# Kernel tuning notes

Hardware: AMD Instinct MI355X
Metric: run time of the kernel (lower is better)

Reference implementation:

```python
import jax, jax.numpy as jnp
import numpy as np

NUM_FEATURES = 602
NUM_CLASSES = 41
HIDDEN = 8
HEADS1 = 8
HEADS2 = 1
N_NODES = 100000
N_EDGES = 1600000
NEG_SLOPE = 0.2  # PyG GATConv default leaky_relu slope
EPS = 1e-16      # PyG softmax denominator epsilon


def gat_conv(x, edge_index, W, att_src, att_dst, bias, heads, out_ch, concat):
    """Faithful PyG GATConv forward (eval mode, dropout disabled).
    x: [N, F_in], edge_index: [2, E] with row0=src, row1=dst.
    W: [F_in, heads*out_ch], att_src/att_dst: [heads, out_ch], bias: [heads*out_ch] or [out_ch].
    """
    N = x.shape[0]
    h = (x @ W).reshape(N, heads, out_ch)              # [N, H, C]
    a_src = jnp.einsum('nhc,hc->nh', h, att_src)       # [N, H]
    a_dst = jnp.einsum('nhc,hc->nh', h, att_dst)       # [N, H]
    src, dst = edge_index[0], edge_index[1]
    e = jax.nn.leaky_relu(a_src[src] + a_dst[dst], NEG_SLOPE)  # [E, H]
    # segment softmax over incoming edges of each dst node
    m = jax.ops.segment_max(e, dst, num_segments=N)    # [N, H]
    e = jnp.exp(e - m[dst])
    denom = jax.ops.segment_sum(e, dst, num_segments=N)  # [N, H]
    alpha = e / (denom[dst] + EPS)                     # [E, H]
    msg = h[src] * alpha[:, :, None]                   # [E, H, C]
    out = jax.ops.segment_sum(msg, dst, num_segments=N)  # [N, H, C]
    if concat:
        out = out.reshape(N, heads * out_ch)
    else:
        out = out.mean(axis=1)
    return out + bias


def setup_inputs() -> dict:
    key = jax.random.key(0)
    ks = jax.random.split(key, 10)
    x = jax.random.normal(ks[0], (N_NODES, NUM_FEATURES), dtype=jnp.float32)
    edge_index = jax.random.randint(ks[1], (2, N_EDGES), 0, N_NODES, dtype=jnp.int64)
    s = 0.1
    W1 = jax.random.normal(ks[2], (NUM_FEATURES, HEADS1 * HIDDEN), dtype=jnp.float32) * s
    att_src1 = jax.random.normal(ks[3], (HEADS1, HIDDEN), dtype=jnp.float32) * s
    att_dst1 = jax.random.normal(ks[4], (HEADS1, HIDDEN), dtype=jnp.float32) * s
    b1 = jnp.zeros((HEADS1 * HIDDEN,), dtype=jnp.float32)
    W2 = jax.random.normal(ks[5], (HEADS1 * HIDDEN, HEADS2 * NUM_CLASSES), dtype=jnp.float32) * s
    att_src2 = jax.random.normal(ks[6], (HEADS2, NUM_CLASSES), dtype=jnp.float32) * s
    att_dst2 = jax.random.normal(ks[7], (HEADS2, NUM_CLASSES), dtype=jnp.float32) * s
    b2 = jnp.zeros((NUM_CLASSES,), dtype=jnp.float32)
    return {"x": x, "edge_index": edge_index, "W1": W1, "att_src1": att_src1,
            "att_dst1": att_dst1, "b1": b1, "W2": W2, "att_src2": att_src2,
            "att_dst2": att_dst2, "b2": b2}


def reference(x, edge_index, W1, att_src1, att_dst1, b1, W2, att_src2, att_dst2, b2):
    # eval mode: all F.dropout calls are identity
    h = gat_conv(x, edge_index, W1, att_src1, att_dst1, b1, HEADS1, HIDDEN, concat=True)
    h = jax.nn.elu(h)
    h = gat_conv(h, edge_index, W2, att_src2, att_dst2, b2, HEADS2, NUM_CLASSES, concat=False)
    return jax.nn.log_softmax(h, axis=1)
```

## Files before the change

kernel.cpp:

```cpp
#include <hip/hip_runtime.h>
#include <math.h>

#define NN 100000
#define NE 1600000
#define F_IN 602
#define H1 8
#define C1 8
#define F_MID 64
#define NC 41
#define H2_LD 48
#define NEG_SLOPE 0.2f
#define WT_LD 640
#define GB1 ((NN + 63) / 64)
#define DGB 1024
#define ATB ((NN * H1 + 255) / 256)

#define LRELU(x) fmaxf((x), NEG_SLOPE * (x))

typedef __attribute__((ext_vector_type(8))) short short8;
typedef __attribute__((ext_vector_type(4))) float f32x4;

__device__ inline unsigned short f2bf(float f) {
    unsigned u = __builtin_bit_cast(unsigned, f);
    unsigned r = (u + 0x7FFFu + ((u >> 16) & 1u)) >> 16;
    return (unsigned short)r;
}
__device__ inline float bf2f(unsigned short u) {
    unsigned v = ((unsigned)u) << 16;
    return __builtin_bit_cast(float, v);
}

__global__ void zero_kernel(int4* __restrict__ p, int n4)
{
    int i = blockIdx.x * blockDim.x + threadIdx.x;
    if (i < n4) p[i] = make_int4(0, 0, 0, 0);
}

__global__ void prep_wt_kernel(const float* __restrict__ W, unsigned short* __restrict__ Wt)
{
    int idx = blockIdx.x * blockDim.x + threadIdx.x;
    if (idx >= F_MID * WT_LD) return;
    int col = idx / WT_LD, k = idx % WT_LD;
    Wt[idx] = (k < F_IN) ? f2bf(W[k * F_MID + col]) : (unsigned short)0;
}

__global__ __launch_bounds__(256) void mega1_kernel(
    const float* __restrict__ x, const unsigned short* __restrict__ Wt,
    unsigned short* __restrict__ h1b,
    const int* __restrict__ dst, int* __restrict__ deg, int* __restrict__ rank,
    int N, int E)
{
    __shared__ unsigned short As[64][40];
    __shared__ unsigned short Bs[64][40];

    int bid = blockIdx.x;
    int t = threadIdx.x;

    if (bid < DGB) {
        for (int e = bid * 256 + t; e < E; e += DGB * 256)
            rank[e] = atomicAdd(&deg[dst[e]], 1);
        return;
    }

    int lane = t & 63;
    int w = t >> 6;
    int l16 = lane & 15, lg = lane >> 4;
    int n0 = (bid - DGB) * 64;

    int arow = t >> 2, aseg = t & 3;
    int grow = n0 + arow;
    const float* xrow = x + (size_t)(grow < N ? grow : 0) * F_IN + aseg * 8;
    int bcol = t >> 2;
    const unsigned short* wrow = Wt + (size_t)bcol * WT_LD + aseg * 8;

    f32x4 acc[4] = {};
    float2 av[4];
    uint4  bv;

    #pragma unroll
    for (int i = 0; i < 4; ++i) av[i] = *(const float2*)(xrow + i * 2);
    bv = *(const uint4*)(wrow);

    for (int kt = 0; kt < 19; ++kt) {
        __syncthreads();
        {
            unsigned short tmp[8];
            #pragma unroll
            for (int i = 0; i < 4; ++i) {
                tmp[i * 2]     = f2bf(av[i].x);
                tmp[i * 2 + 1] = f2bf(av[i].y);
            }
            *(uint4*)(&As[arow][aseg * 8]) = *(uint4*)tmp;
            *(uint4*)(&Bs[bcol][aseg * 8]) = bv;
        }
        __syncthreads();

        if (kt < 18) {
            int k0 = (kt + 1) * 32;
            if (kt + 1 < 18) {
                #pragma unroll
                for (int i = 0; i < 4; ++i) av[i] = *(const float2*)(xrow + k0 + i * 2);
            } else {
                #pragma unroll
                for (int i = 0; i < 4; ++i) {
                    int k = k0 + aseg * 8 + i * 2;
                    float a = (k < F_IN)     ? xrow[k0 + i * 2]     : 0.f;
                    float b = (k + 1 < F_IN) ? xrow[k0 + i * 2 + 1] : 0.f;
                    av[i] = make_float2(a, b);
                }
            }
            bv = *(const uint4*)(wrow + k0);
        }

        short8 afrag = *(const short8*)(&As[w * 16 + l16][lg * 8]);
        short8 bfrag[4];
        #pragma unroll
        for (int n = 0; n < 4; ++n)
            bfrag[n] = *(const short8*)(&Bs[n * 16 + l16][lg * 8]);
        #pragma unroll
        for (int n = 0; n < 4; ++n)
            acc[n] = __builtin_amdgcn_mfma_f32_16x16x32_bf16(afrag, bfrag[n], acc[n], 0, 0, 0);
    }

    #pragma unroll
    for (int r = 0; r < 4; ++r) {
        int row = n0 + w * 16 + lg * 4 + r;
        if (row < N) {
            #pragma unroll
            for (int n = 0; n < 4; ++n)
                h1b[(size_t)row * F_MID + n * 16 + l16] = f2bf(acc[n][r]);
        }
    }
}

__global__ void scan1_kernel(const int* __restrict__ deg, int* __restrict__ bsum, int N)
{
    int b = blockIdx.x, t = threadIdx.x;
    int base = b * 1024 + t * 16;
    int s = 0;
    #pragma unroll
    for (int i = 0; i < 16; ++i) { int idx = base + i; if (idx < N) s += deg[idx]; }
    #pragma unroll
    for (int o = 32; o > 0; o >>= 1) s += __shfl_down(s, o);
    if (t == 0) bsum[b] = s;
}

__global__ void scan2_kernel(const int* __restrict__ bsum, int* __restrict__ boff,
                             int nb, int* __restrict__ offs, int N, int E)
{
    __shared__ int buf[128];
    int t = threadIdx.x;
    int v = (t < nb) ? bsum[t] : 0;
    buf[t] = v;
    __syncthreads();
    for (int o = 1; o < 128; o <<= 1) {
        int u = (t >= o) ? buf[t - o] : 0;
        __syncthreads();
        buf[t] += u;
        __syncthreads();
    }
    if (t < nb) boff[t] = buf[t] - v;
    if (t == 0) offs[N] = E;
}

__global__ void scan3_kernel(const int* __restrict__ deg, const int* __restrict__ boff,
                             int* __restrict__ offs, int N)
{
    int b = blockIdx.x, t = threadIdx.x;
    int base = b * 1024 + t * 16;
    int loc[16];
    int s = 0;
    #pragma unroll
    for (int i = 0; i < 16; ++i) {
        int idx = base + i;
        loc[i] = (idx < N) ? deg[idx] : 0;
        s += loc[i];
    }
    int inc = s;
    #pragma unroll
    for (int o = 1; o < 64; o <<= 1) {
        int u = __shfl_up(inc, o);
        if (t >= o) inc += u;
    }
    int run = inc - s + boff[b];
    #pragma unroll
    for (int i = 0; i < 16; ++i) {
        int idx = base + i;
        if (idx < N) offs[idx] = run;
        run += loc[i];
    }
}

__global__ void mega2_kernel(
    const unsigned short* __restrict__ h1b,
    const float* __restrict__ attS, const float* __restrict__ attD,
    float* __restrict__ asrc, float* __restrict__ adst,
    const int* __restrict__ src, const int* __restrict__ dst,
    const int* __restrict__ rank, const int* __restrict__ offs,
    int* __restrict__ srcs, int N, int E)
{
    int bid = blockIdx.x, t = threadIdx.x;
    if (bid < DGB) {
        for (int e = bid * 256 + t; e < E; e += DGB * 256)
            srcs[offs[dst[e]] + rank[e]] = src[e];
        return;
    }
    int idx = (bid - DGB) * 256 + t;
    if (idx >= N * H1) return;
    int n = idx >> 3, hh = idx & 7;
    float s = 0.f, d = 0.f;
    #pragma unroll
    for (int c = 0; c < C1; ++c) {
        float v = bf2f(h1b[n * F_MID + hh * C1 + c]);
        s += v * attS[hh * C1 + c];
        d += v * attD[hh * C1 + c];
    }
    asrc[idx] = s;
    adst[idx] = d;
}

__global__ void agg1_kernel(const int* __restrict__ offs, const int* __restrict__ srcs,
                            const unsigned short* __restrict__ h1b,
                            const float* __restrict__ asrc, const float* __restrict__ adst,
                            const float* __restrict__ b1,
                            float* __restrict__ out1, int N)
{
    int wave = (blockIdx.x * blockDim.x + threadIdx.x) >> 6;
    int lane = threadIdx.x & 63;
    if (wave >= N) return;
    int n = wave;
    int hh = lane >> 3;
    int beg = offs[n], end = offs[n + 1];
    float ad = adst[n * H1 + hh];

    float m = -INFINITY, den = 0.f, acc = 0.f;
    int i = beg;
    for (; i + 8 <= end; i += 8) {
        int s[8];
        #pragma unroll
        for (int j = 0; j < 8; ++j) s[j] = srcs[i + j];
        float a[8], v[8];
        #pragma unroll
        for (int j = 0; j < 8; ++j) a[j] = asrc[s[j] * H1 + hh];
        #pragma unroll
        for (int j = 0; j < 8; ++j) v[j] = bf2f(h1b[(size_t)s[j] * F_MID + lane]);
        float e[8];
        #pragma unroll
        for (int j = 0; j < 8; ++j) e[j] = LRELU(a[j] + ad);
        float m8 = fmaxf(fmaxf(fmaxf(e[0], e[1]), fmaxf(e[2], e[3])),
                         fmaxf(fmaxf(e[4], e[5]), fmaxf(e[6], e[7])));
        float mn = fmaxf(m, m8);
        float sc = __expf(m - mn);
        float p[8];
        #pragma unroll
        for (int j = 0; j < 8; ++j) p[j] = __expf(e[j] - mn);
        den = den * sc + (((p[0] + p[1]) + (p[2] + p[3])) + ((p[4] + p[5]) + (p[6] + p[7])));
        acc = acc * sc + (((p[0] * v[0] + p[1] * v[1]) + (p[2] * v[2] + p[3] * v[3]))
                        + ((p[4] * v[4] + p[5] * v[5]) + (p[6] * v[6] + p[7] * v[7])));
        m = mn;
    }
    for (; i < end; ++i) {
        int s = srcs[i];
        float e = LRELU(asrc[s * H1 + hh] + ad);
        float hv = bf2f(h1b[(size_t)s * F_MID + lane]);
        float mn = fmaxf(m, e);
        float sc = __expf(m - mn);
        float p  = __expf(e - mn);
        den = den * sc + p;
        acc = acc * sc + p * hv;
        m = mn;
    }
    float inv = 1.f / (den + 1e-16f);
    float v = acc * inv + b1[lane];
    out1[n * F_MID + lane] = v > 0.f ? v : expm1f(v);
}

__global__ __launch_bounds__(256) void gemm2_kernel(
    const float* __restrict__ out1, const float* __restrict__ W2,
    float* __restrict__ h2p, int N)
{
    __shared__ float ws[F_MID * NC];
    for (int i = threadIdx.x; i < F_MID * NC; i += 256) ws[i] = W2[i];
    __syncthreads();
    int idx = blockIdx.x * blockDim.x + threadIdx.x;
    if (idx >= N * NC) return;
    int n = idx / NC, j = idx % NC;
    const float* row = out1 + n * F_MID;
    float acc = 0.f;
    #pragma unroll
    for (int k = 0; k < F_MID; ++k) acc += row[k] * ws[k * NC + j];
    h2p[(size_t)n * H2_LD + j] = acc;
}

__global__ void attn2_kernel(float* __restrict__ h2p,
                             const float* __restrict__ attS,
                             const float* __restrict__ attD,
                             float* __restrict__ adst, int N)
{
    int n = blockIdx.x * blockDim.x + threadIdx.x;
    if (n >= N) return;
    float s = 0.f, d = 0.f;
    #pragma unroll
    for (int j = 0; j < NC; ++j) {
        float v = h2p[(size_t)n * H2_LD + j];
        s += v * attS[j];
        d += v * attD[j];
    }
    h2p[(size_t)n * H2_LD + NC] = s;
    adst[n] = d;
}

__global__ void agg2_kernel(const int* __restrict__ offs, const int* __restrict__ srcs,
                            const float* __restrict__ h2p,
                            const float* __restrict__ adst,
                            const float* __restrict__ b2,
                            float* __restrict__ out, int N)
{
    int wave = (blockIdx.x * blockDim.x + threadIdx.x) >> 6;
    int lane = threadIdx.x & 63;
    if (wave >= N) return;
    int n = wave;
    int beg = offs[n], end = offs[n + 1];
    float ad = adst[n];
    bool act = lane < NC;
    int li = act ? lane : NC;

    float m = -INFINITY, den = 0.f, acc = 0.f;
    int i = beg;
    for (; i + 8 <= end; i += 8) {
        int s[8];
        #pragma unroll
        for (int j = 0; j < 8; ++j) s[j] = srcs[i + j];
        float hv[8];
        #pragma unroll
        for (int j = 0; j < 8; ++j) hv[j] = h2p[(size_t)s[j] * H2_LD + li];
        float a[8];
        #pragma unroll
        for (int j = 0; j < 8; ++j) a[j] = __shfl(hv[j], NC);
        float e[8];
        #pragma unroll
        for (int j = 0; j < 8; ++j) e[j] = LRELU(a[j] + ad);
        float m8 = fmaxf(fmaxf(fmaxf(e[0], e[1]), fmaxf(e[2], e[3])),
                         fmaxf(fmaxf(e[4], e[5]), fmaxf(e[6], e[7])));
        float mn = fmaxf(m, m8);
        float sc = __expf(m - mn);
        float p[8];
        #pragma unroll
        for (int j = 0; j < 8; ++j) p[j] = __expf(e[j] - mn);
        den = den * sc + (((p[0] + p[1]) + (p[2] + p[3])) + ((p[4] + p[5]) + (p[6] + p[7])));
        acc = acc * sc + (((p[0] * hv[0] + p[1] * hv[1]) + (p[2] * hv[2] + p[3] * hv[3]))
                        + ((p[4] * hv[4] + p[5] * hv[5]) + (p[6] * hv[6] + p[7] * hv[7])));
        m = mn;
    }
    for (; i < end; ++i) {
        int s = srcs[i];
        float hv = h2p[(size_t)s * H2_LD + li];
        float a = __shfl(hv, NC);
        float e = LRELU(a + ad);
        float mn = fmaxf(m, e);
        float sc = __expf(m - mn);
        float p  = __expf(e - mn);
        den = den * sc + p;
        acc = acc * sc + p * hv;
        m = mn;
    }
    float inv = 1.f / (den + 1e-16f);
    float v = act ? acc * inv + b2[lane] : -INFINITY;
    float mm = v;
    #pragma unroll
    for (int o = 32; o > 0; o >>= 1) mm = fmaxf(mm, __shfl_xor(mm, o));
    float ex = act ? __expf(v - mm) : 0.f;
    float S = ex;
    #pragma unroll
    for (int o = 32; o > 0; o >>= 1) S += __shfl_xor(S, o);
    if (act) out[n * NC + lane] = v - mm - logf(S);
}

extern "C" void kernel_launch(void* const* d_in, const int* in_sizes, int n_in,
                              void* d_out, int out_size, void* d_ws, size_t ws_size,
                              hipStream_t stream)
{
    const float* x     = (const float*)d_in[0];
    const int*   ei    = (const int*)  d_in[1];
    const float* W1    = (const float*)d_in[2];
    const float* attS1 = (const float*)d_in[3];
    const float* attD1 = (const float*)d_in[4];
    const float* b1    = (const float*)d_in[5];
    const float* W2    = (const float*)d_in[6];
    const float* attS2 = (const float*)d_in[7];
    const float* attD2 = (const float*)d_in[8];
    const float* b2    = (const float*)d_in[9];
    float* out = (float*)d_out;

    const int N = NN, E = NE;
    const int* src = ei;
    const int* dst = ei + E;

    char* p = (char*)d_ws;
    auto alloc = [&](size_t bytes) { char* r = p; p += (bytes + 255) & ~255ull; return r; };
    unsigned short* h1b = (unsigned short*)alloc((size_t)N * F_MID * 2);
    float* asrc1 = (float*)alloc((size_t)N * H1 * 4);
    float* adst1 = (float*)alloc((size_t)N * H1 * 4);
    float* out1  = (float*)alloc((size_t)N * F_MID * 4);
    float* h2p   = (float*)alloc((size_t)N * H2_LD * 4);
    float* adst2 = (float*)alloc((size_t)N * 4);
    int*   deg   = (int*)alloc((size_t)N * 4);
    int*   rank  = (int*)alloc((size_t)E * 4);
    int*   offs  = (int*)alloc((size_t)(N + 1) * 4);
    int*   srcs  = (int*)alloc((size_t)E * 4);
    unsigned short* Wt = (unsigned short*)alloc((size_t)F_MID * WT_LD * 2);
    const int NB = (N + 1023) / 1024;
    int*   bsum  = (int*)alloc((size_t)NB * 4);
    int*   boff  = (int*)alloc((size_t)NB * 4);

    zero_kernel<<<(N / 4 + 255) / 256, 256, 0, stream>>>((int4*)deg, N / 4);
    prep_wt_kernel<<<(F_MID * WT_LD + 255) / 256, 256, 0, stream>>>(W1, Wt);
    mega1_kernel<<<DGB + GB1, 256, 0, stream>>>(x, Wt, h1b, dst, deg, rank, N, E);
    scan1_kernel<<<NB, 64, 0, stream>>>(deg, bsum, N);
    scan2_kernel<<<1, 128, 0, stream>>>(bsum, boff, NB, offs, N, E);
    scan3_kernel<<<NB, 64, 0, stream>>>(deg, boff, offs, N);
    mega2_kernel<<<DGB + ATB, 256, 0, stream>>>(
        h1b, attS1, attD1, asrc1, adst1, src, dst, rank, offs, srcs, N, E);
    agg1_kernel<<<(N * 64 + 255) / 256, 256, 0, stream>>>(
        offs, srcs, h1b, asrc1, adst1, b1, out1, N);
    gemm2_kernel<<<(N * NC + 255) / 256, 256, 0, stream>>>(out1, W2, h2p, N);
    attn2_kernel<<<(N + 255) / 256, 256, 0, stream>>>(h2p, attS2, attD2, adst2, N);
    agg2_kernel<<<(N * 64 + 255) / 256, 256, 0, stream>>>(offs, srcs, h2p, adst2, b2, out, N);
}
```

Measured before the change: 409.8 us.

## Load GEMM fragments directly from global memory, dropping LDS staging and barriers

The first-layer x@W GEMM no longer stages A and B tiles through shared memory with two barriers per k-step. Each lane now loads its MFMA fragments straight from global memory (x as fp32, converted to bf16 in registers; Wt as bf16) inside a fully unrolled k loop. This removes LDS traffic and synchronisation, but each wave now reloads the whole Wt slice from global/L2, and the A loads are less coalesced because each lane reads 32 bytes from its own row.

```diff
diff --git a/kernel.cpp b/kernel.cpp
--- a/kernel.cpp
+++ b/kernel.cpp
@@ -29,6 +29,18 @@
     unsigned v = ((unsigned)u) << 16;
     return __builtin_bit_cast(float, v);
 }
+__device__ inline short8 load_cvt8(const float* __restrict__ p) {
+    float2 v0 = *(const float2*)(p);
+    float2 v1 = *(const float2*)(p + 2);
+    float2 v2 = *(const float2*)(p + 4);
+    float2 v3 = *(const float2*)(p + 6);
+    short8 r;
+    r[0] = (short)f2bf(v0.x); r[1] = (short)f2bf(v0.y);
+    r[2] = (short)f2bf(v1.x); r[3] = (short)f2bf(v1.y);
+    r[4] = (short)f2bf(v2.x); r[5] = (short)f2bf(v2.y);
+    r[6] = (short)f2bf(v3.x); r[7] = (short)f2bf(v3.y);
+    return r;
+}
 
 __global__ void zero_kernel(int4* __restrict__ p, int n4)
 {
@@ -50,9 +62,6 @@
     const int* __restrict__ dst, int* __restrict__ deg, int* __restrict__ rank,
     int N, int E)
 {
-    __shared__ unsigned short As[64][40];
-    __shared__ unsigned short Bs[64][40];
-
     int bid = blockIdx.x;
     int t = threadIdx.x;
 
@@ -65,70 +74,53 @@
     int lane = t & 63;
     int w = t >> 6;
     int l16 = lane & 15, lg = lane >> 4;
-    int n0 = (bid - DGB) * 64;
-
-    int arow = t >> 2, aseg = t & 3;
-    int grow = n0 + arow;
-    const float* xrow = x + (size_t)(grow < N ? grow : 0) * F_IN + aseg * 8;
-    int bcol = t >> 2;
-    const unsigned short* wrow = Wt + (size_t)bcol * WT_LD + aseg * 8;
+    int row0 = (bid - DGB) * 64 + w * 16;
+
+    int r = row0 + l16;
+    const float* a = x + (size_t)(r < N ? r : 0) * F_IN + lg * 8;
+    const unsigned short* bp = Wt + (size_t)l16 * WT_LD + lg * 8;
 
     f32x4 acc[4] = {};
-    float2 av[4];
-    uint4  bv;
-
-    #pragma unroll
-    for (int i = 0; i < 4; ++i) av[i] = *(const float2*)(xrow + i * 2);
-    bv = *(const uint4*)(wrow);
-
-    for (int kt = 0; kt < 19; ++kt) {
-        __syncthreads();
-        {
-            unsigned short tmp[8];
-            #pragma unroll
-            for (int i = 0; i < 4; ++i) {
-                tmp[i * 2]     = f2bf(av[i].x);
-                tmp[i * 2 + 1] = f2bf(av[i].y);
-            }
-            *(uint4*)(&As[arow][aseg * 8]) = *(uint4*)tmp;
-            *(uint4*)(&Bs[bcol][aseg * 8]) = bv;
+
+    #pragma unroll
+    for (int kt = 0; kt < 18; ++kt) {
+        int ko = kt * 32;
+        short8 af = load_cvt8(a + ko);
+        short8 bf[4];
+        #pragma unroll
+        for (int n = 0; n < 4; ++n)
+            bf[n] = *(const short8*)(bp + (size_t)n * 16 * WT_LD + ko);
+        #pragma unroll
+        for (int n = 0; n < 4; ++n)
+            acc[n] = __builtin_amdgcn_mfma_f32_16x16x32_bf16(af, bf[n], acc[n], 0, 0, 0);
+    }
+    {
+        const int ko = 576;
+        float v[8];
+        #pragma unroll
+        for (int i = 0; i < 8; ++i) {
+            int k = ko + lg * 8 + i;
+            v[i] = (k < F_IN) ? a[ko + i] : 0.f;
         }
-        __syncthreads();
-
-        if (kt < 18) {
-            int k0 = (kt + 1) * 32;
-            if (kt + 1 < 18) {
-                #pragma unroll
-                for (int i = 0; i < 4; ++i) av[i] = *(const float2*)(xrow + k0 + i * 2);
-            } else {
-                #pragma unroll
-                for (int i = 0; i < 4; ++i) {
-                    int k = k0 + aseg * 8 + i * 2;
-                    float a = (k < F_IN)     ? xrow[k0 + i * 2]     : 0.f;
-                    float b = (k + 1 < F_IN) ? xrow[k0 + i * 2 + 1] : 0.f;
-                    av[i] = make_float2(a, b);
-                }
-            }
-            bv = *(const uint4*)(wrow + k0);
-        }
-
-        short8 afrag = *(const short8*)(&As[w * 16 + l16][lg * 8]);
-        short8 bfrag[4];
+        short8 af;
+        #pragma unroll
+        for (int i = 0; i < 8; ++i) af[i] = (short)f2bf(v[i]);
+        short8 bf[4];
         #pragma unroll
         for (int n = 0; n < 4; ++n)
-            bfrag[n] = *(const short8*)(&Bs[n * 16 + l16][lg * 8]);
+            bf[n] = *(const short8*)(bp + (size_t)n * 16 * WT_LD + ko);
         #pragma unroll
         for (int n = 0; n < 4; ++n)
-            acc[n] = __builtin_amdgcn_mfma_f32_16x16x32_bf16(afrag, bfrag[n], acc[n], 0, 0, 0);
-    }
-
-    #pragma unroll
-    for (int r = 0; r < 4; ++r) {
-        int row = n0 + w * 16 + lg * 4 + r;
+            acc[n] = __builtin_amdgcn_mfma_f32_16x16x32_bf16(af, bf[n], acc[n], 0, 0, 0);
+    }
+
+    #pragma unroll
+    for (int rr = 0; rr < 4; ++rr) {
+        int row = row0 + lg * 4 + rr;
         if (row < N) {
             #pragma unroll
             for (int n = 0; n < 4; ++n)
-                h1b[(size_t)row * F_MID + n * 16 + l16] = f2bf(acc[n][r]);
+                h1b[(size_t)row * F_MID + n * 16 + l16] = f2bf(acc[n][rr]);
         }
     }
 }
```

Result: slower. 445.1 us (+8.6%).
